# Kernel optimization log

Hardware: AMD Instinct MI355X
Metric: run time of the kernel (lower is better)

## Reference

```python
import jax, jax.numpy as jnp
import numpy as np

D_MODEL = 1280
N_HEADS = 16
DEPTH = D_MODEL // N_HEADS  # 80
NEG_BIG = -10000.0


def setup_inputs() -> dict:
    key = jax.random.key(0)
    ks = jax.random.split(key, 12)
    B, S = 2, 2048
    std = 1.0 / np.sqrt(D_MODEL)
    inp = {
        "v": jax.random.normal(ks[0], (B, S, D_MODEL), jnp.float32),
        "k": jax.random.normal(ks[1], (B, S, D_MODEL), jnp.float32),
        "q": jax.random.normal(ks[2], (B, S, D_MODEL), jnp.float32),
        # causal mask: 1.0 on strictly-upper triangle (future positions)
        "mask": jnp.triu(jnp.ones((S, S), jnp.float32), k=1),
        "Wq_w": jax.random.normal(ks[3], (D_MODEL, D_MODEL), jnp.float32) * std,
        "Wq_b": jnp.zeros((D_MODEL,), jnp.float32),
        "Wk_w": jax.random.normal(ks[4], (D_MODEL, D_MODEL), jnp.float32) * std,
        "Wk_b": jnp.zeros((D_MODEL,), jnp.float32),
        "Wv_w": jax.random.normal(ks[5], (D_MODEL, D_MODEL), jnp.float32) * std,
        "Wv_b": jnp.zeros((D_MODEL,), jnp.float32),
        "dense_w": jax.random.normal(ks[6], (D_MODEL, D_MODEL), jnp.float32) * std,
        "dense_b": jnp.zeros((D_MODEL,), jnp.float32),
    }
    return inp


def _split_heads(x, B):
    # [B, S, D] -> [B, H, S, depth]
    return x.reshape(B, -1, N_HEADS, DEPTH).transpose(0, 2, 1, 3)


def reference(v, k, q, mask, Wq_w, Wq_b, Wk_w, Wk_b, Wv_w, Wv_b, dense_w, dense_b):
    B = q.shape[0]
    # torch Linear: y = x @ W.T + b
    qh = _split_heads(q @ Wq_w.T + Wq_b, B)
    kh = _split_heads(k @ Wk_w.T + Wk_b, B)
    vh = _split_heads(v @ Wv_w.T + Wv_b, B)

    scale = 1.0 / np.sqrt(DEPTH)
    logits = jnp.einsum("bhqd,bhkd->bhqk", qh, kh) * scale  # [B,H,S,S]
    nd, ns = logits.shape[-2], logits.shape[-1]
    logits = logits + mask[ns - nd:ns, :ns] * NEG_BIG
    attn = jax.nn.softmax(logits, axis=-1)
    out = jnp.einsum("bhqk,bhkd->bhqd", attn, vh)  # [B,H,S,depth]
    out = out.transpose(0, 2, 1, 3).reshape(B, -1, D_MODEL)
    out = out @ dense_w.T + dense_b
    return out, attn
```

## Files before the change

### kernel.cpp

```cpp
#include <hip/hip_runtime.h>
#include <hip/hip_bf16.h>

typedef short frag8 __attribute__((ext_vector_type(8)));
typedef float facc4 __attribute__((ext_vector_type(4)));
typedef float f32x4 __attribute__((ext_vector_type(4)));
typedef unsigned short ushort_t;
typedef unsigned int uint_t;

#define DEV static __device__ __forceinline__

DEV ushort_t f2bf(float f) {
  uint_t u = __float_as_uint(f);
  u += 0x7fffu + ((u >> 16) & 1u);
  return (ushort_t)(u >> 16);
}
DEV uint_t cvt_pk(float lo, float hi) {
  uint_t r;
  asm("v_cvt_pk_bf16_f32 %0, %1, %2" : "=v"(r) : "v"(lo), "v"(hi));
  return r;
}
DEV frag8 pack8(float4 a, float4 b) {
  union { frag8 f; uint4 u; } u_;
  u_.u.x = cvt_pk(a.x, a.y); u_.u.y = cvt_pk(a.z, a.w);
  u_.u.z = cvt_pk(b.x, b.y); u_.u.w = cvt_pk(b.z, b.w);
  return u_.f;
}
DEV void bar_lds() { asm volatile("s_waitcnt lgkmcnt(0)\n\ts_barrier" ::: "memory"); }

constexpr int B_ = 2, S_ = 2048, H_ = 16, DM = 1280, DH = 80, DP = 96;
constexpr size_t IN_E = (size_t)B_ * S_ * DM;
constexpr size_t WT_E = (size_t)DM * DM;
constexpr size_t OFF_WQ = 0;
constexpr size_t OFF_WK = OFF_WQ + WT_E;
constexpr size_t OFF_WV = OFF_WK + WT_E;
constexpr size_t OFF_WD = OFF_WV + WT_E;
constexpr size_t QH_E  = (size_t)B_ * H_ * S_ * DP;
constexpr size_t OFF_QH = OFF_WD + WT_E;
constexpr size_t OFF_KH = OFF_QH + QH_E;
constexpr size_t VT_E  = (size_t)B_ * H_ * DH * S_;
constexpr size_t OFF_VT = OFF_KH + QH_E;
constexpr size_t OFF_OH = OFF_VT + VT_E;

constexpr float QSCALE = 0.16129822f;

__global__ void convert_kernel(const float* __restrict__ wq, const float* __restrict__ wk,
                               const float* __restrict__ wv, const float* __restrict__ wd,
                               ushort_t* __restrict__ ws) {
  size_t i = (size_t)blockIdx.x * blockDim.x + threadIdx.x;
  size_t stride = (size_t)gridDim.x * blockDim.x;
  constexpr size_t TOTAL = 4 * WT_E / 8;
  constexpr size_t NROW = (size_t)B_ * H_ * S_;
  constexpr size_t PADC = 2 * NROW * 2;
  for (size_t c = i; c < TOTAL + PADC; c += stride) {
    if (c < TOTAL) {
      size_t e = c * 8;
      const float* s2; size_t lo;
      if      (e < WT_E)     { s2 = wq; lo = e; }
      else if (e < 2 * WT_E) { s2 = wk; lo = e - WT_E; }
      else if (e < 3 * WT_E) { s2 = wv; lo = e - 2 * WT_E; }
      else                   { s2 = wd; lo = e - 3 * WT_E; }
      float4 a = *(const float4*)(s2 + lo);
      float4 b = *(const float4*)(s2 + lo + 4);
      uint4 o;
      o.x = (uint_t)f2bf(a.x) | ((uint_t)f2bf(a.y) << 16);
      o.y = (uint_t)f2bf(a.z) | ((uint_t)f2bf(a.w) << 16);
      o.z = (uint_t)f2bf(b.x) | ((uint_t)f2bf(b.y) << 16);
      o.w = (uint_t)f2bf(b.z) | ((uint_t)f2bf(b.w) << 16);
      *(uint4*)(ws + e) = o;
    } else {
      size_t rr = c - TOTAL;
      size_t row = rr >> 1;
      size_t base = (row < NROW ? OFF_QH : OFF_KH) + (row & (NROW - 1)) * DP + DH + (rr & 1) * 8;
      uint4 z = {0u, 0u, 0u, 0u};
      *(uint4*)(ws + base) = z;
    }
  }
}

__global__ __launch_bounds__(256) void qkv_kernel(const float* __restrict__ Aq,
                                                  const float* __restrict__ Ak,
                                                  const float* __restrict__ Av,
                                                  const ushort_t* __restrict__ wts,
                                                  const float* __restrict__ bq,
                                                  const float* __restrict__ bk,
                                                  const float* __restrict__ bv,
                                                  ushort_t* __restrict__ qh_o,
                                                  ushort_t* __restrict__ kh_o,
                                                  ushort_t* __restrict__ vt_o) {
  __shared__ __align__(16) ushort_t sA[2][128][40];
  __shared__ __align__(16) ushort_t sB[2][128][40];
  int which = blockIdx.x / 320;
  int local = blockIdx.x - which * 320;
  int swz = (local & 7) * 40 + (local >> 3);
  int tm = swz / 10, tn = swz % 10;
  int m0 = tm * 128, n0 = tn * 128;
  const float* A = which == 0 ? Aq : which == 1 ? Ak : Av;
  const ushort_t* W = wts + (size_t)which * WT_E;
  const float* bias = which == 0 ? bq : which == 1 ? bk : bv;
  int tid = threadIdx.x, l = tid & 63, wv = tid >> 6;
  int lm = l & 15, lg = l >> 4;
  int wr = wv >> 1, wc = wv & 1;
  int srow = tid >> 2, schk = tid & 3;
  facc4 acc[4][4] = {};
  frag8 ra[2], rb[2];

  auto load_tile = [&](int kt) {
    const float* Ab = A + (size_t)(m0 + srow) * DM + kt * 32 + schk * 8;
    ra[0] = pack8(*(const float4*)Ab, *(const float4*)(Ab + 4));
    const float* Ab2 = Ab + (size_t)64 * DM;
    ra[1] = pack8(*(const float4*)Ab2, *(const float4*)(Ab2 + 4));
    const ushort_t* Bb = W + (size_t)(n0 + srow) * DM + kt * 32 + schk * 8;
    rb[0] = *(const frag8*)Bb;
    rb[1] = *(const frag8*)(Bb + (size_t)64 * DM);
  };
  auto store_tile = [&](int bb) {
    *(frag8*)&sA[bb][srow][schk * 8] = ra[0];
    *(frag8*)&sA[bb][srow + 64][schk * 8] = ra[1];
    *(frag8*)&sB[bb][srow][schk * 8] = rb[0];
    *(frag8*)&sB[bb][srow + 64][schk * 8] = rb[1];
  };

  load_tile(0);
  store_tile(0);
  __syncthreads();
  for (int kt = 0; kt < 40; ++kt) {
    int cur = kt & 1;
    if (kt < 39) load_tile(kt + 1);
    frag8 af[4], bf[4];
#pragma unroll
    for (int i = 0; i < 4; ++i) af[i] = *(const frag8*)&sA[cur][wr * 64 + i * 16 + lm][lg * 8];
#pragma unroll
    for (int i = 0; i < 4; ++i) bf[i] = *(const frag8*)&sB[cur][wc * 64 + i * 16 + lm][lg * 8];
#pragma unroll
    for (int mi = 0; mi < 4; ++mi)
#pragma unroll
      for (int ni = 0; ni < 4; ++ni)
        acc[mi][ni] = __builtin_amdgcn_mfma_f32_16x16x32_bf16(af[mi], bf[ni], acc[mi][ni], 0, 0, 0);
    if (kt < 39) store_tile(cur ^ 1);
    __syncthreads();
  }

  float scale = (which == 0) ? QSCALE : 1.0f;
  ushort_t* dst = which == 0 ? qh_o : which == 1 ? kh_o : vt_o;
#pragma unroll
  for (int ni = 0; ni < 4; ++ni) {
    int n = n0 + wc * 64 + ni * 16 + lm;
    float bv2 = bias[n];
    int h = n / 80, d = n % 80;
#pragma unroll
    for (int mi = 0; mi < 4; ++mi) {
      int mbase = m0 + wr * 64 + mi * 16 + lg * 4;
      int b = mbase >> 11, sp = mbase & 2047;
      if (which < 2) {
#pragma unroll
        for (int r = 0; r < 4; ++r) {
          float vl = (acc[mi][ni][r] + bv2) * scale;
          dst[((size_t)(b * H_ + h) * S_ + sp + r) * DP + d] = f2bf(vl);
        }
      } else {
        uint2 u2;
        u2.x = cvt_pk(acc[mi][ni][0] + bv2, acc[mi][ni][1] + bv2);
        u2.y = cvt_pk(acc[mi][ni][2] + bv2, acc[mi][ni][3] + bv2);
        *(uint2*)&dst[((size_t)(b * H_ + h) * DH + d) * S_ + sp] = u2;
      }
    }
  }
}

__global__ __launch_bounds__(256) void dense_kernel(const ushort_t* __restrict__ A,
                                                    const ushort_t* __restrict__ W,
                                                    const float* __restrict__ bias,
                                                    float* __restrict__ dst_f) {
  __shared__ __align__(16) ushort_t sA[2][128][40];
  __shared__ __align__(16) ushort_t sB[2][128][40];
  int bid = blockIdx.x;
  int swz = (bid & 7) * 40 + (bid >> 3);
  int tm = swz / 10, tn = swz % 10;
  int m0 = tm * 128, n0 = tn * 128;
  int tid = threadIdx.x, l = tid & 63, wv = tid >> 6;
  int lm = l & 15, lg = l >> 4;
  int wr = wv >> 1, wc = wv & 1;
  int srow = tid >> 2, schk = tid & 3;
  facc4 acc[4][4] = {};
  frag8 ra[2], rb[2];

  auto load_tile = [&](int kt) {
    const ushort_t* Ab = A + (size_t)(m0 + srow) * DM + kt * 32 + schk * 8;
    ra[0] = *(const frag8*)Ab;
    ra[1] = *(const frag8*)(Ab + (size_t)64 * DM);
    const ushort_t* Bb = W + (size_t)(n0 + srow) * DM + kt * 32 + schk * 8;
    rb[0] = *(const frag8*)Bb;
    rb[1] = *(const frag8*)(Bb + (size_t)64 * DM);
  };
  auto store_tile = [&](int bb) {
    *(frag8*)&sA[bb][srow][schk * 8] = ra[0];
    *(frag8*)&sA[bb][srow + 64][schk * 8] = ra[1];
    *(frag8*)&sB[bb][srow][schk * 8] = rb[0];
    *(frag8*)&sB[bb][srow + 64][schk * 8] = rb[1];
  };

  load_tile(0);
  store_tile(0);
  __syncthreads();
  for (int kt = 0; kt < 40; ++kt) {
    int cur = kt & 1;
    if (kt < 39) load_tile(kt + 1);
    frag8 af[4], bf[4];
#pragma unroll
    for (int i = 0; i < 4; ++i) af[i] = *(const frag8*)&sA[cur][wr * 64 + i * 16 + lm][lg * 8];
#pragma unroll
    for (int i = 0; i < 4; ++i) bf[i] = *(const frag8*)&sB[cur][wc * 64 + i * 16 + lm][lg * 8];
#pragma unroll
    for (int mi = 0; mi < 4; ++mi)
#pragma unroll
      for (int ni = 0; ni < 4; ++ni)
        acc[mi][ni] = __builtin_amdgcn_mfma_f32_16x16x32_bf16(af[mi], bf[ni], acc[mi][ni], 0, 0, 0);
    if (kt < 39) store_tile(cur ^ 1);
    __syncthreads();
  }

#pragma unroll
  for (int ni = 0; ni < 4; ++ni) {
    int n = n0 + wc * 64 + ni * 16 + lm;
    float bv2 = bias[n];
#pragma unroll
    for (int mi = 0; mi < 4; ++mi) {
      int mbase = m0 + wr * 64 + mi * 16 + lg * 4;
#pragma unroll
      for (int r = 0; r < 4; ++r)
        __builtin_nontemporal_store(acc[mi][ni][r] + bv2, dst_f + (size_t)(mbase + r) * DM + n);
    }
  }
}

__global__ __launch_bounds__(512, 4) void attn_kernel(const ushort_t* __restrict__ qh,
                                                      const ushort_t* __restrict__ kh,
                                                      const ushort_t* __restrict__ vt,
                                                      ushort_t* __restrict__ outh,
                                                      float* __restrict__ out_attn) {
  __shared__ __align__(16) ushort_t sK[2][64][104];
  __shared__ __align__(16) ushort_t sV[2][80][68];
  __shared__ __align__(16) char sP[8 * 2048];
  int bid = blockIdx.x;
  int half = bid >> 8, rr0 = bid & 255;
  int swz = (rr0 & 7) * 32 + (rr0 >> 3);
  int bh = swz >> 3, pr = swz & 7;
  int b = bh >> 4, h = bh & 15;
  int s = half ? (15 - pr) : pr;
  int tid = threadIdx.x, w = tid >> 6, l = tid & 63, lm = l & 15, lg = l >> 4;
  const ushort_t* qhb = qh + (size_t)bh * S_ * DP;
  const ushort_t* khb = kh + (size_t)bh * S_ * DP;
  const ushort_t* vtb = vt + (size_t)bh * DH * S_;
  float* attnb = out_attn + (size_t)bh * S_ * S_;
  char* Pw = sP + w * 2048;

  int sr[3], sc[3];
#pragma unroll
  for (int i = 0; i < 3; ++i) {
    int c = tid * 3 + i;
    sr[i] = c / 24; sc[i] = (c % 24) * 4;
  }
  uint2 stk[3];
  auto ldtK = [&](int t) {
#pragma unroll
    for (int i = 0; i < 3; ++i)
      stk[i] = *(const uint2*)(khb + (size_t)(t * 64 + sr[i]) * DP + sc[i]);
  };
  auto sttK = [&](int bb) {
#pragma unroll
    for (int i = 0; i < 3; ++i)
      *(uint2*)&sK[bb][sr[i]][sc[i]] = stk[i];
  };
  int vrow = tid >> 3, vcol = (tid & 7) * 8;
  uint4 stv0, stv1;
  auto ldtV = [&](int t) {
    stv0 = *(const uint4*)(vtb + (size_t)vrow * S_ + t * 64 + vcol);
    if (tid < 128) stv1 = *(const uint4*)(vtb + (size_t)(64 + vrow) * S_ + t * 64 + vcol);
  };
  auto sttV = [&](int bb) {
    *(uint4*)&sV[bb][vrow][vcol] = stv0;
    if (tid < 128) *(uint4*)&sV[bb][64 + vrow][vcol] = stv1;
  };

  int q0 = s * 128;
  int wq0 = q0 + w * 16;
  int qg = wq0 + lm;

  if (s < 15) {
    int c0 = (s + 1) * 128;
    int r2 = tid >> 2;
    int l4 = (tid & 3) << 2;
    float* rowp = attnb + (size_t)(q0 + r2) * S_ + c0 + l4;
    f32x4 z = {0.f, 0.f, 0.f, 0.f};
    for (int cc = 0; cc < 2048 - c0; cc += 16)
      __builtin_nontemporal_store(z, (f32x4*)(rowp + cc));
  }

  frag8 qf[3];
#pragma unroll
  for (int kd = 0; kd < 3; ++kd)
    qf[kd] = *(const frag8*)(qhb + (size_t)qg * DP + kd * 32 + lg * 8);
  int NT = 2 * (s + 1);

  float rs4[4] = {0.f, 0.f, 0.f, 0.f};
  ldtK(0); sttK(0);
  if (NT > 1) ldtK(1);
  bar_lds();
  for (int t = 0; t < NT; ++t) {
    int cur = t & 1;
    if (t + 1 < NT) sttK(cur ^ 1);
    if (t + 2 < NT) ldtK(t + 2);
    if (64 * t < wq0 + 16) {
      facc4 acc[4] = {};
#pragma unroll
      for (int mi = 0; mi < 4; ++mi)
#pragma unroll
        for (int kd = 0; kd < 3; ++kd) {
          frag8 af = *(const frag8*)((const char*)sK + cur * (64 * 104 * 2) +
                                     (mi * 16 + lm) * 208 + kd * 64 + lg * 16);
          acc[mi] = __builtin_amdgcn_mfma_f32_16x16x32_bf16(af, qf[kd], acc[mi], 0, 0, 0);
        }
      if (64 * t + 63 <= wq0) {
#pragma unroll
        for (int mi = 0; mi < 4; ++mi)
#pragma unroll
          for (int r = 0; r < 4; ++r) rs4[r] += exp2f(acc[mi][r]);
      } else {
#pragma unroll
        for (int mi = 0; mi < 4; ++mi)
#pragma unroll
          for (int r = 0; r < 4; ++r) {
            int kg = t * 64 + mi * 16 + lg * 4 + r;
            if (kg <= qg) rs4[r] += exp2f(acc[mi][r]);
          }
      }
    }
    bar_lds();
  }
  float rs = (rs4[0] + rs4[1]) + (rs4[2] + rs4[3]);
  rs += __shfl_xor(rs, 16);
  rs += __shfl_xor(rs, 32);
  float li = -__log2f(rs);

  facc4 acc2[5] = {};
  ldtK(0); ldtV(0); sttK(0); sttV(0);
  if (NT > 1) { ldtK(1); ldtV(1); }
  bar_lds();
  for (int t = 0; t < NT; ++t) {
    int cur = t & 1;
    if (t + 1 < NT) { sttK(cur ^ 1); sttV(cur ^ 1); }
    if (t + 2 < NT) { ldtK(t + 2); ldtV(t + 2); }
    if (64 * t >= wq0 + 16) {
      f32x4 z = {0.f, 0.f, 0.f, 0.f};
#pragma unroll
      for (int mi = 0; mi < 4; ++mi)
        *(f32x4*)(attnb + (size_t)qg * S_ + t * 64 + mi * 16 + lg * 4) = z;
    } else {
      facc4 acc[4] = {};
#pragma unroll
      for (int mi = 0; mi < 4; ++mi)
#pragma unroll
        for (int kd = 0; kd < 3; ++kd) {
          frag8 af = *(const frag8*)((const char*)sK + cur * (64 * 104 * 2) +
                                     (mi * 16 + lm) * 208 + kd * 64 + lg * 16);
          acc[mi] = __builtin_amdgcn_mfma_f32_16x16x32_bf16(af, qf[kd], acc[mi], 0, 0, 0);
        }
      bool full = (64 * t + 63 <= wq0);
#pragma unroll
      for (int mi = 0; mi < 4; ++mi) {
        float p[4];
        if (full) {
#pragma unroll
          for (int r = 0; r < 4; ++r) p[r] = exp2f(acc[mi][r] + li);
        } else {
#pragma unroll
          for (int r = 0; r < 4; ++r) {
            int kg = t * 64 + mi * 16 + lg * 4 + r;
            p[r] = (kg <= qg) ? exp2f(acc[mi][r] + li) : 0.f;
          }
        }
        f32x4 f4 = {p[0], p[1], p[2], p[3]};
        *(f32x4*)(attnb + (size_t)qg * S_ + t * 64 + mi * 16 + lg * 4) = f4;
        uint2 pk;
        pk.x = cvt_pk(p[0], p[1]);
        pk.y = cvt_pk(p[2], p[3]);
        int kb = mi * 32 + lg * 8;
        *(uint2*)(Pw + lm * 128 + (kb ^ ((lm & 7) << 4))) = pk;
      }
#pragma unroll
      for (int ks = 0; ks < 2; ++ks) {
        int kbyte = ks * 64 + lg * 16;
        frag8 pa = *(const frag8*)(Pw + lm * 128 + (kbyte ^ ((lm & 7) << 4)));
#pragma unroll
        for (int nf = 0; nf < 5; ++nf) {
          frag8 vb = *(const frag8*)&sV[cur][nf * 16 + lm][ks * 32 + lg * 8];
          acc2[nf] = __builtin_amdgcn_mfma_f32_16x16x32_bf16(pa, vb, acc2[nf], 0, 0, 0);
        }
      }
    }
    bar_lds();
  }
#pragma unroll
  for (int nf = 0; nf < 5; ++nf)
#pragma unroll
    for (int r = 0; r < 4; ++r) {
      int qrow = q0 + w * 16 + lg * 4 + r;
      int col = h * DH + nf * 16 + lm;
      outh[((size_t)b * S_ + qrow) * DM + col] = f2bf(acc2[nf][r]);
    }
}

extern "C" void kernel_launch(void* const* d_in, const int* in_sizes, int n_in,
                              void* d_out, int out_size, void* d_ws, size_t ws_size,
                              hipStream_t stream) {
  const float* v  = (const float*)d_in[0];
  const float* k  = (const float*)d_in[1];
  const float* q  = (const float*)d_in[2];
  const float* wq = (const float*)d_in[4];
  const float* bq = (const float*)d_in[5];
  const float* wk = (const float*)d_in[6];
  const float* bk = (const float*)d_in[7];
  const float* wv = (const float*)d_in[8];
  const float* bv = (const float*)d_in[9];
  const float* wd = (const float*)d_in[10];
  const float* bd = (const float*)d_in[11];
  ushort_t* ws = (ushort_t*)d_ws;
  float* out  = (float*)d_out;
  float* attn = out + IN_E;

  convert_kernel<<<2048, 256, 0, stream>>>(wq, wk, wv, wd, ws);
  qkv_kernel<<<960, 256, 0, stream>>>(q, k, v, ws + OFF_WQ, bq, bk, bv,
                                      ws + OFF_QH, ws + OFF_KH, ws + OFF_VT);
  attn_kernel<<<512, 512, 0, stream>>>(ws + OFF_QH, ws + OFF_KH, ws + OFF_VT, ws + OFF_OH, attn);
  dense_kernel<<<320, 256, 0, stream>>>(ws + OFF_OH, ws + OFF_WD, bd, out);
}
```

Measured before the change: 353.2 us.

## Fuse weight conversion into GEMMs and restructure attention K/V pipeline

```diff
diff --git a/kernel.cpp b/kernel.cpp
--- a/kernel.cpp
+++ b/kernel.cpp
@@ -30,12 +30,8 @@
 constexpr int B_ = 2, S_ = 2048, H_ = 16, DM = 1280, DH = 80, DP = 96;
 constexpr size_t IN_E = (size_t)B_ * S_ * DM;
 constexpr size_t WT_E = (size_t)DM * DM;
-constexpr size_t OFF_WQ = 0;
-constexpr size_t OFF_WK = OFF_WQ + WT_E;
-constexpr size_t OFF_WV = OFF_WK + WT_E;
-constexpr size_t OFF_WD = OFF_WV + WT_E;
 constexpr size_t QH_E  = (size_t)B_ * H_ * S_ * DP;
-constexpr size_t OFF_QH = OFF_WD + WT_E;
+constexpr size_t OFF_QH = 0;
 constexpr size_t OFF_KH = OFF_QH + QH_E;
 constexpr size_t VT_E  = (size_t)B_ * H_ * DH * S_;
 constexpr size_t OFF_VT = OFF_KH + QH_E;
@@ -43,44 +39,21 @@
 
 constexpr float QSCALE = 0.16129822f;
 
-__global__ void convert_kernel(const float* __restrict__ wq, const float* __restrict__ wk,
-                               const float* __restrict__ wv, const float* __restrict__ wd,
-                               ushort_t* __restrict__ ws) {
-  size_t i = (size_t)blockIdx.x * blockDim.x + threadIdx.x;
-  size_t stride = (size_t)gridDim.x * blockDim.x;
-  constexpr size_t TOTAL = 4 * WT_E / 8;
+__global__ void pad_kernel(ushort_t* __restrict__ ws) {
   constexpr size_t NROW = (size_t)B_ * H_ * S_;
-  constexpr size_t PADC = 2 * NROW * 2;
-  for (size_t c = i; c < TOTAL + PADC; c += stride) {
-    if (c < TOTAL) {
-      size_t e = c * 8;
-      const float* s2; size_t lo;
-      if      (e < WT_E)     { s2 = wq; lo = e; }
-      else if (e < 2 * WT_E) { s2 = wk; lo = e - WT_E; }
-      else if (e < 3 * WT_E) { s2 = wv; lo = e - 2 * WT_E; }
-      else                   { s2 = wd; lo = e - 3 * WT_E; }
-      float4 a = *(const float4*)(s2 + lo);
-      float4 b = *(const float4*)(s2 + lo + 4);
-      uint4 o;
-      o.x = (uint_t)f2bf(a.x) | ((uint_t)f2bf(a.y) << 16);
-      o.y = (uint_t)f2bf(a.z) | ((uint_t)f2bf(a.w) << 16);
-      o.z = (uint_t)f2bf(b.x) | ((uint_t)f2bf(b.y) << 16);
-      o.w = (uint_t)f2bf(b.z) | ((uint_t)f2bf(b.w) << 16);
-      *(uint4*)(ws + e) = o;
-    } else {
-      size_t rr = c - TOTAL;
-      size_t row = rr >> 1;
-      size_t base = (row < NROW ? OFF_QH : OFF_KH) + (row & (NROW - 1)) * DP + DH + (rr & 1) * 8;
-      uint4 z = {0u, 0u, 0u, 0u};
-      *(uint4*)(ws + base) = z;
-    }
-  }
+  size_t c = (size_t)blockIdx.x * blockDim.x + threadIdx.x;
+  size_t row = c >> 1;
+  size_t base = (row < NROW ? OFF_QH : OFF_KH) + (row & (NROW - 1)) * DP + DH + (c & 1) * 8;
+  uint4 z = {0u, 0u, 0u, 0u};
+  *(uint4*)(ws + base) = z;
 }
 
 __global__ __launch_bounds__(256) void qkv_kernel(const float* __restrict__ Aq,
                                                   const float* __restrict__ Ak,
                                                   const float* __restrict__ Av,
-                                                  const ushort_t* __restrict__ wts,
+                                                  const float* __restrict__ Wq,
+                                                  const float* __restrict__ Wk,
+                                                  const float* __restrict__ Wv,
                                                   const float* __restrict__ bq,
                                                   const float* __restrict__ bk,
                                                   const float* __restrict__ bv,
@@ -95,7 +68,7 @@
   int tm = swz / 10, tn = swz % 10;
   int m0 = tm * 128, n0 = tn * 128;
   const float* A = which == 0 ? Aq : which == 1 ? Ak : Av;
-  const ushort_t* W = wts + (size_t)which * WT_E;
+  const float* W = which == 0 ? Wq : which == 1 ? Wk : Wv;
   const float* bias = which == 0 ? bq : which == 1 ? bk : bv;
   int tid = threadIdx.x, l = tid & 63, wv = tid >> 6;
   int lm = l & 15, lg = l >> 4;
@@ -109,9 +82,10 @@
     ra[0] = pack8(*(const float4*)Ab, *(const float4*)(Ab + 4));
     const float* Ab2 = Ab + (size_t)64 * DM;
     ra[1] = pack8(*(const float4*)Ab2, *(const float4*)(Ab2 + 4));
-    const ushort_t* Bb = W + (size_t)(n0 + srow) * DM + kt * 32 + schk * 8;
-    rb[0] = *(const frag8*)Bb;
-    rb[1] = *(const frag8*)(Bb + (size_t)64 * DM);
+    const float* Bb = W + (size_t)(n0 + srow) * DM + kt * 32 + schk * 8;
+    rb[0] = pack8(*(const float4*)Bb, *(const float4*)(Bb + 4));
+    const float* Bb2 = Bb + (size_t)64 * DM;
+    rb[1] = pack8(*(const float4*)Bb2, *(const float4*)(Bb2 + 4));
   };
   auto store_tile = [&](int bb) {
     *(frag8*)&sA[bb][srow][schk * 8] = ra[0];
@@ -168,7 +142,7 @@
 }
 
 __global__ __launch_bounds__(256) void dense_kernel(const ushort_t* __restrict__ A,
-                                                    const ushort_t* __restrict__ W,
+                                                    const float* __restrict__ W,
                                                     const float* __restrict__ bias,
                                                     float* __restrict__ dst_f) {
   __shared__ __align__(16) ushort_t sA[2][128][40];
@@ -188,9 +162,10 @@
     const ushort_t* Ab = A + (size_t)(m0 + srow) * DM + kt * 32 + schk * 8;
     ra[0] = *(const frag8*)Ab;
     ra[1] = *(const frag8*)(Ab + (size_t)64 * DM);
-    const ushort_t* Bb = W + (size_t)(n0 + srow) * DM + kt * 32 + schk * 8;
-    rb[0] = *(const frag8*)Bb;
-    rb[1] = *(const frag8*)(Bb + (size_t)64 * DM);
+    const float* Bb = W + (size_t)(n0 + srow) * DM + kt * 32 + schk * 8;
+    rb[0] = pack8(*(const float4*)Bb, *(const float4*)(Bb + 4));
+    const float* Bb2 = Bb + (size_t)64 * DM;
+    rb[1] = pack8(*(const float4*)Bb2, *(const float4*)(Bb2 + 4));
   };
   auto store_tile = [&](int bb) {
     *(frag8*)&sA[bb][srow][schk * 8] = ra[0];
@@ -260,26 +235,24 @@
     int c = tid * 3 + i;
     sr[i] = c / 24; sc[i] = (c % 24) * 4;
   }
-  uint2 stk[3];
-  auto ldtK = [&](int t) {
+  auto ldK = [&](int t, uint2* r) {
 #pragma unroll
     for (int i = 0; i < 3; ++i)
-      stk[i] = *(const uint2*)(khb + (size_t)(t * 64 + sr[i]) * DP + sc[i]);
-  };
-  auto sttK = [&](int bb) {
+      r[i] = *(const uint2*)(khb + (size_t)(t * 64 + sr[i]) * DP + sc[i]);
+  };
+  auto stK = [&](int bb, const uint2* r) {
 #pragma unroll
     for (int i = 0; i < 3; ++i)
-      *(uint2*)&sK[bb][sr[i]][sc[i]] = stk[i];
+      *(uint2*)&sK[bb][sr[i]][sc[i]] = r[i];
   };
   int vrow = tid >> 3, vcol = (tid & 7) * 8;
-  uint4 stv0, stv1;
-  auto ldtV = [&](int t) {
-    stv0 = *(const uint4*)(vtb + (size_t)vrow * S_ + t * 64 + vcol);
-    if (tid < 128) stv1 = *(const uint4*)(vtb + (size_t)(64 + vrow) * S_ + t * 64 + vcol);
-  };
-  auto sttV = [&](int bb) {
-    *(uint4*)&sV[bb][vrow][vcol] = stv0;
-    if (tid < 128) *(uint4*)&sV[bb][64 + vrow][vcol] = stv1;
+  auto ldV = [&](int t, uint4* r) {
+    r[0] = *(const uint4*)(vtb + (size_t)vrow * S_ + t * 64 + vcol);
+    if (tid < 128) r[1] = *(const uint4*)(vtb + (size_t)(64 + vrow) * S_ + t * 64 + vcol);
+  };
+  auto stV = [&](int bb, const uint4* r) {
+    *(uint4*)&sV[bb][vrow][vcol] = r[0];
+    if (tid < 128) *(uint4*)&sV[bb][64 + vrow][vcol] = r[1];
   };
 
   int q0 = s * 128;
@@ -303,39 +276,53 @@
   int NT = 2 * (s + 1);
 
   float rs4[4] = {0.f, 0.f, 0.f, 0.f};
-  ldtK(0); sttK(0);
-  if (NT > 1) ldtK(1);
-  bar_lds();
-  for (int t = 0; t < NT; ++t) {
-    int cur = t & 1;
-    if (t + 1 < NT) sttK(cur ^ 1);
-    if (t + 2 < NT) ldtK(t + 2);
-    if (64 * t < wq0 + 16) {
-      facc4 acc[4] = {};
+  auto comp1 = [&](int bb, int t) {
+    if (64 * t >= wq0 + 16) return;
+    facc4 acc[4] = {};
+    __builtin_amdgcn_s_setprio(1);
+#pragma unroll
+    for (int mi = 0; mi < 4; ++mi)
+#pragma unroll
+      for (int kd = 0; kd < 3; ++kd) {
+        frag8 af = *(const frag8*)((const char*)sK + bb * (64 * 104 * 2) +
+                                   (mi * 16 + lm) * 208 + kd * 64 + lg * 16);
+        acc[mi] = __builtin_amdgcn_mfma_f32_16x16x32_bf16(af, qf[kd], acc[mi], 0, 0, 0);
+      }
+    __builtin_amdgcn_s_setprio(0);
+    if (64 * t + 63 <= wq0) {
 #pragma unroll
       for (int mi = 0; mi < 4; ++mi)
 #pragma unroll
-        for (int kd = 0; kd < 3; ++kd) {
-          frag8 af = *(const frag8*)((const char*)sK + cur * (64 * 104 * 2) +
-                                     (mi * 16 + lm) * 208 + kd * 64 + lg * 16);
-          acc[mi] = __builtin_amdgcn_mfma_f32_16x16x32_bf16(af, qf[kd], acc[mi], 0, 0, 0);
+        for (int r = 0; r < 4; ++r) rs4[r] += exp2f(acc[mi][r]);
+    } else {
+#pragma unroll
+      for (int mi = 0; mi < 4; ++mi)
+#pragma unroll
+        for (int r = 0; r < 4; ++r) {
+          int kg = t * 64 + mi * 16 + lg * 4 + r;
+          if (kg <= qg) rs4[r] += exp2f(acc[mi][r]);
         }
-      if (64 * t + 63 <= wq0) {
-#pragma unroll
-        for (int mi = 0; mi < 4; ++mi)
-#pragma unroll
-          for (int r = 0; r < 4; ++r) rs4[r] += exp2f(acc[mi][r]);
-      } else {
-#pragma unroll
-        for (int mi = 0; mi < 4; ++mi)
-#pragma unroll
-          for (int r = 0; r < 4; ++r) {
-            int kg = t * 64 + mi * 16 + lg * 4 + r;
-            if (kg <= qg) rs4[r] += exp2f(acc[mi][r]);
-          }
-      }
-    }
+    }
+  };
+  {
+    uint2 rka[3], rkb[3];
+    ldK(0, rka); ldK(1, rkb);
+    stK(0, rka);
+    if (NT > 2) ldK(2, rka);
     bar_lds();
+    for (int j = 0; j < NT / 2; ++j) {
+      int t0 = 2 * j, t1 = t0 + 1;
+      stK(1, rkb);
+      if (t1 + 2 < NT) ldK(t1 + 2, rkb);
+      comp1(0, t0);
+      bar_lds();
+      if (t0 + 2 < NT) {
+        stK(0, rka);
+        if (t0 + 4 < NT) ldK(t0 + 4, rka);
+      }
+      comp1(1, t1);
+      bar_lds();
+    }
   }
   float rs = (rs4[0] + rs4[1]) + (rs4[2] + rs4[3]);
   rs += __shfl_xor(rs, 16);
@@ -343,62 +330,80 @@
   float li = -__log2f(rs);
 
   facc4 acc2[5] = {};
-  ldtK(0); ldtV(0); sttK(0); sttV(0);
-  if (NT > 1) { ldtK(1); ldtV(1); }
-  bar_lds();
-  for (int t = 0; t < NT; ++t) {
-    int cur = t & 1;
-    if (t + 1 < NT) { sttK(cur ^ 1); sttV(cur ^ 1); }
-    if (t + 2 < NT) { ldtK(t + 2); ldtV(t + 2); }
+  auto comp2 = [&](int bb, int t) {
     if (64 * t >= wq0 + 16) {
       f32x4 z = {0.f, 0.f, 0.f, 0.f};
 #pragma unroll
       for (int mi = 0; mi < 4; ++mi)
         *(f32x4*)(attnb + (size_t)qg * S_ + t * 64 + mi * 16 + lg * 4) = z;
-    } else {
-      facc4 acc[4] = {};
-#pragma unroll
-      for (int mi = 0; mi < 4; ++mi)
-#pragma unroll
-        for (int kd = 0; kd < 3; ++kd) {
-          frag8 af = *(const frag8*)((const char*)sK + cur * (64 * 104 * 2) +
-                                     (mi * 16 + lm) * 208 + kd * 64 + lg * 16);
-          acc[mi] = __builtin_amdgcn_mfma_f32_16x16x32_bf16(af, qf[kd], acc[mi], 0, 0, 0);
+      return;
+    }
+    facc4 acc[4] = {};
+    __builtin_amdgcn_s_setprio(1);
+#pragma unroll
+    for (int mi = 0; mi < 4; ++mi)
+#pragma unroll
+      for (int kd = 0; kd < 3; ++kd) {
+        frag8 af = *(const frag8*)((const char*)sK + bb * (64 * 104 * 2) +
+                                   (mi * 16 + lm) * 208 + kd * 64 + lg * 16);
+        acc[mi] = __builtin_amdgcn_mfma_f32_16x16x32_bf16(af, qf[kd], acc[mi], 0, 0, 0);
+      }
+    __builtin_amdgcn_s_setprio(0);
+    bool full = (64 * t + 63 <= wq0);
+#pragma unroll
+    for (int mi = 0; mi < 4; ++mi) {
+      float p[4];
+      if (full) {
+#pragma unroll
+        for (int r = 0; r < 4; ++r) p[r] = exp2f(acc[mi][r] + li);
+      } else {
+#pragma unroll
+        for (int r = 0; r < 4; ++r) {
+          int kg = t * 64 + mi * 16 + lg * 4 + r;
+          p[r] = (kg <= qg) ? exp2f(acc[mi][r] + li) : 0.f;
         }
-      bool full = (64 * t + 63 <= wq0);
-#pragma unroll
-      for (int mi = 0; mi < 4; ++mi) {
-        float p[4];
-        if (full) {
-#pragma unroll
-          for (int r = 0; r < 4; ++r) p[r] = exp2f(acc[mi][r] + li);
-        } else {
-#pragma unroll
-          for (int r = 0; r < 4; ++r) {
-            int kg = t * 64 + mi * 16 + lg * 4 + r;
-            p[r] = (kg <= qg) ? exp2f(acc[mi][r] + li) : 0.f;
-          }
-        }
-        f32x4 f4 = {p[0], p[1], p[2], p[3]};
-        *(f32x4*)(attnb + (size_t)qg * S_ + t * 64 + mi * 16 + lg * 4) = f4;
-        uint2 pk;
-        pk.x = cvt_pk(p[0], p[1]);
-        pk.y = cvt_pk(p[2], p[3]);
-        int kb = mi * 32 + lg * 8;
-        *(uint2*)(Pw + lm * 128 + (kb ^ ((lm & 7) << 4))) = pk;
-      }
-#pragma unroll
-      for (int ks = 0; ks < 2; ++ks) {
-        int kbyte = ks * 64 + lg * 16;
-        frag8 pa = *(const frag8*)(Pw + lm * 128 + (kbyte ^ ((lm & 7) << 4)));
-#pragma unroll
-        for (int nf = 0; nf < 5; ++nf) {
-          frag8 vb = *(const frag8*)&sV[cur][nf * 16 + lm][ks * 32 + lg * 8];
-          acc2[nf] = __builtin_amdgcn_mfma_f32_16x16x32_bf16(pa, vb, acc2[nf], 0, 0, 0);
-        }
-      }
-    }
+      }
+      f32x4 f4 = {p[0], p[1], p[2], p[3]};
+      *(f32x4*)(attnb + (size_t)qg * S_ + t * 64 + mi * 16 + lg * 4) = f4;
+      uint2 pk;
+      pk.x = cvt_pk(p[0], p[1]);
+      pk.y = cvt_pk(p[2], p[3]);
+      int kb = mi * 32 + lg * 8;
+      *(uint2*)(Pw + lm * 128 + (kb ^ ((lm & 7) << 4))) = pk;
+    }
+    __builtin_amdgcn_s_setprio(1);
+#pragma unroll
+    for (int ks = 0; ks < 2; ++ks) {
+      int kbyte = ks * 64 + lg * 16;
+      frag8 pa = *(const frag8*)(Pw + lm * 128 + (kbyte ^ ((lm & 7) << 4)));
+#pragma unroll
+      for (int nf = 0; nf < 5; ++nf) {
+        frag8 vb = *(const frag8*)&sV[bb][nf * 16 + lm][ks * 32 + lg * 8];
+        acc2[nf] = __builtin_amdgcn_mfma_f32_16x16x32_bf16(pa, vb, acc2[nf], 0, 0, 0);
+      }
+    }
+    __builtin_amdgcn_s_setprio(0);
+  };
+  {
+    uint2 rka[3], rkb[3];
+    uint4 rva[2], rvb[2];
+    ldK(0, rka); ldV(0, rva); ldK(1, rkb); ldV(1, rvb);
+    stK(0, rka); stV(0, rva);
+    if (NT > 2) { ldK(2, rka); ldV(2, rva); }
     bar_lds();
+    for (int j = 0; j < NT / 2; ++j) {
+      int t0 = 2 * j, t1 = t0 + 1;
+      stK(1, rkb); stV(1, rvb);
+      if (t1 + 2 < NT) { ldK(t1 + 2, rkb); ldV(t1 + 2, rvb); }
+      comp2(0, t0);
+      bar_lds();
+      if (t0 + 2 < NT) {
+        stK(0, rka); stV(0, rva);
+        if (t0 + 4 < NT) { ldK(t0 + 4, rka); ldV(t0 + 4, rva); }
+      }
+      comp2(1, t1);
+      bar_lds();
+    }
   }
 #pragma unroll
   for (int nf = 0; nf < 5; ++nf)
@@ -428,9 +433,9 @@
   float* out  = (float*)d_out;
   float* attn = out + IN_E;
 
-  convert_kernel<<<2048, 256, 0, stream>>>(wq, wk, wv, wd, ws);
-  qkv_kernel<<<960, 256, 0, stream>>>(q, k, v, ws + OFF_WQ, bq, bk, bv,
+  pad_kernel<<<1024, 256, 0, stream>>>(ws);
+  qkv_kernel<<<960, 256, 0, stream>>>(q, k, v, wq, wk, wv, bq, bk, bv,
                                       ws + OFF_QH, ws + OFF_KH, ws + OFF_VT);
   attn_kernel<<<512, 512, 0, stream>>>(ws + OFF_QH, ws + OFF_KH, ws + OFF_VT, ws + OFF_OH, attn);
-  dense_kernel<<<320, 256, 0, stream>>>(ws + OFF_OH, ws + OFF_WD, bd, out);
-}
+  dense_kernel<<<320, 256, 0, stream>>>(ws + OFF_OH, wd, bd, out);
+}
```

After: 380.1 us. 1.08x slower.
